# Performance work log

Hardware: AMD Instinct MI355X
Metric: run time of the kernel (lower is better)

Reference implementation:

```python
import jax, jax.numpy as jnp
import numpy as np

N_NODES = 50000
N_EDGES = 800000
D_IN = 128
D_OUT = 128


def _dedup_mask(src, dst, n_nodes):
    # True for exactly one representative edge per unique (src, dst) pair.
    # Equivalent to the torch unique() over cat(src_feat, dst) rows, since
    # distinct src nodes have distinct (random continuous) feature rows.
    key = src.astype(jnp.int64) * n_nodes + dst.astype(jnp.int64)
    order = jnp.argsort(key)
    ks = key[order]
    first = jnp.concatenate([jnp.array([True]), ks[1:] != ks[:-1]])
    mask = jnp.zeros(key.shape[0], dtype=bool).at[order].set(first)
    return mask


def setup_inputs() -> dict:
    key = jax.random.key(0)
    k1, k2, k3, k4, k5, k6, k7 = jax.random.split(key, 7)
    nfeats = jax.random.normal(k1, (N_NODES, D_IN), dtype=jnp.float32)
    src = jax.random.randint(k2, (N_EDGES,), 0, N_NODES, dtype=jnp.int64)
    dst = jax.random.randint(k3, (N_EDGES,), 0, N_NODES, dtype=jnp.int64)
    s1 = 1.0 / np.sqrt(D_IN)
    s2 = 1.0 / np.sqrt(D_OUT)
    W1 = jax.random.uniform(k4, (D_IN, D_OUT), jnp.float32, -s1, s1)
    b1 = jax.random.uniform(k5, (D_OUT,), jnp.float32, -s1, s1)
    W2 = jax.random.uniform(k6, (D_OUT, D_OUT), jnp.float32, -s2, s2)
    b2 = jax.random.uniform(k7, (D_OUT,), jnp.float32, -s2, s2)
    alpha = jnp.zeros((1,), dtype=jnp.float32)  # init_alpha=0, not learned
    return {"nfeats": nfeats, "src": src, "dst": dst,
            "W1": W1, "b1": b1, "W2": W2, "b2": b2, "alpha": alpha}


def reference(nfeats, src, dst, W1, b1, W2, b2, alpha):
    # message: gather src features, zero out duplicate (feat, dst) rows
    mask = _dedup_mask(src, dst, N_NODES)  # [E]
    m = nfeats[src] * mask[:, None].astype(nfeats.dtype)  # [E, D_IN]
    # sum aggregation into dst nodes
    agg = jax.ops.segment_sum(m, dst, num_segments=N_NODES)  # [N, D_IN]
    h = (1.0 + alpha[0]) * nfeats + agg
    # MLP (2 layers): Linear -> ReLU -> Linear (BatchNorms unused in source forward)
    h = jax.nn.relu(h @ W1 + b1)
    h = h @ W2 + b2
    # norm=None, act=None, dropout=0 -> identity
    return h
```

## Files before the change

### kernel.cpp

```cpp
#include <hip/hip_runtime.h>

typedef unsigned int u32;
typedef unsigned short u16;
typedef long long i64;

#define NNODES 50000
#define NEDGES 800000
#define DF 128
#define CAP 64
#define NBINS 196
#define BINCAP 5120
#define EPB 4096

typedef __bf16 bf16x8 __attribute__((ext_vector_type(8)));
typedef float f32x4 __attribute__((ext_vector_type(4)));

__device__ __forceinline__ u16 f2bf(float f) {
    union { float f; u32 i; } v; v.f = f;
    u32 u = v.i;
    return (u16)((u + 0x7fffu + ((u >> 16) & 1u)) >> 16);
}

__global__ __launch_bounds__(256) void detect_kernel(const u32* __restrict__ src_w,
                                                     u32* __restrict__ flag,
                                                     u32* __restrict__ cursors) {
    __shared__ int any_nz;
    cursors[threadIdx.x] = 0u;
    if (threadIdx.x == 0) any_nz = 0;
    __syncthreads();
    if (src_w[2 * threadIdx.x + 1] != 0u) atomicOr(&any_nz, 1);
    __syncthreads();
    if (threadIdx.x == 0) *flag = (any_nz == 0) ? 1u : 0u;
}

__global__ __launch_bounds__(256) void bin_kernel(const void* __restrict__ src,
                                                  const void* __restrict__ dst,
                                                  const u32* __restrict__ flag,
                                                  u32* __restrict__ cursors,
                                                  u32* __restrict__ binbuf) {
    __shared__ u32 s_cnt[NBINS];
    __shared__ u32 s_base[NBINS];
    int t = threadIdx.x;
    for (int i = t; i < NBINS; i += 256) s_cnt[i] = 0u;
    __syncthreads();

    bool is64 = (*flag != 0u);
    int e0 = blockIdx.x * EPB + t;
    u32 pk[16];
#pragma unroll
    for (int i = 0; i < 16; ++i) {
        int e = e0 + i * 256;
        pk[i] = 0xFFFFFFFFu;
        if (e < NEDGES) {
            int s, d;
            if (is64) { s = (int)((const i64*)src)[e]; d = (int)((const i64*)dst)[e]; }
            else      { s = ((const int*)src)[e];      d = ((const int*)dst)[e]; }
            pk[i] = (u32)s | ((u32)d << 16);
            atomicAdd(&s_cnt[(u32)d >> 8], 1u);
        }
    }
    __syncthreads();
    if (t < NBINS) {
        s_base[t] = atomicAdd(&cursors[t], s_cnt[t]);
        s_cnt[t] = 0u;
    }
    __syncthreads();
#pragma unroll
    for (int i = 0; i < 16; ++i) {
        if (pk[i] != 0xFFFFFFFFu) {
            u32 bin = pk[i] >> 24;
            u32 off = s_base[bin] + atomicAdd(&s_cnt[bin], 1u);
            if (off < BINCAP) binbuf[bin * BINCAP + off] = pk[i];
        }
    }
}

__global__ __launch_bounds__(256) void build_kernel(const u32* __restrict__ cursors,
                                                    const u32* __restrict__ binbuf,
                                                    u32* __restrict__ counts,
                                                    int* __restrict__ edge_src) {
    __shared__ u32 cnt[256];
    int t = threadIdx.x;
    cnt[t] = 0u;
    __syncthreads();
    int b = blockIdx.x;
    int n = (int)cursors[b]; if (n > BINCAP) n = BINCAP;
    for (int i = t; i < n; i += 256) {
        u32 pk = binbuf[b * BINCAP + i];
        int srcv = (int)(pk & 0xFFFFu);
        int dl = (int)((pk >> 16) & 0xFFu);
        u32 pos = atomicAdd(&cnt[dl], 1u);
        if (pos < CAP) edge_src[(((b << 8) + dl) << 6) + (int)pos] = srcv;
    }
    __syncthreads();
    counts[(b << 8) + t] = cnt[t];
}

__global__ __launch_bounds__(256) void gather_kernel(const float* __restrict__ nf,
                                                     const u32* __restrict__ counts,
                                                     const int* __restrict__ edge_src,
                                                     const float* __restrict__ alpha,
                                                     u16* __restrict__ X) {
    __shared__ __align__(16) int s_kept[4][CAP];
    int w = threadIdx.x >> 6, lane = threadIdx.x & 63;
    int d = blockIdx.x * 4 + w;
    int c = (int)counts[d];
    int cc = c < CAP ? c : CAP;

    float al = 1.0f + alpha[0];
    float2 dv = *(const float2*)(nf + (size_t)d * DF + 2 * lane);

    int si = 0;
    bool k = false;
    if (lane < cc) { si = edge_src[(d << 6) + lane]; k = true; }
    for (int j = 0; j < cc - 1; ++j) {
        int v = __shfl(si, j, 64);
        if (j < lane && v == si) k = false;
    }
    unsigned long long m = __ballot(k);
    if (k) s_kept[w][__popcll(m & ((1ull << lane) - 1ull))] = si;
    int nk = __popcll(m);
    __builtin_amdgcn_wave_barrier();

    float a0 = 0.f, a1 = 0.f;
    int i = 0;
    for (; i + 8 <= nk; i += 8) {
        int4 q0 = *(const int4*)&s_kept[w][i];
        int4 q1 = *(const int4*)&s_kept[w][i + 4];
        float2 v0 = *(const float2*)(nf + (size_t)q0.x * DF + 2 * lane);
        float2 v1 = *(const float2*)(nf + (size_t)q0.y * DF + 2 * lane);
        float2 v2 = *(const float2*)(nf + (size_t)q0.z * DF + 2 * lane);
        float2 v3 = *(const float2*)(nf + (size_t)q0.w * DF + 2 * lane);
        float2 v4 = *(const float2*)(nf + (size_t)q1.x * DF + 2 * lane);
        float2 v5 = *(const float2*)(nf + (size_t)q1.y * DF + 2 * lane);
        float2 v6 = *(const float2*)(nf + (size_t)q1.z * DF + 2 * lane);
        float2 v7 = *(const float2*)(nf + (size_t)q1.w * DF + 2 * lane);
        a0 += ((v0.x + v1.x) + (v2.x + v3.x)) + ((v4.x + v5.x) + (v6.x + v7.x));
        a1 += ((v0.y + v1.y) + (v2.y + v3.y)) + ((v4.y + v5.y) + (v6.y + v7.y));
    }
    for (; i + 4 <= nk; i += 4) {
        int4 q = *(const int4*)&s_kept[w][i];
        float2 v0 = *(const float2*)(nf + (size_t)q.x * DF + 2 * lane);
        float2 v1 = *(const float2*)(nf + (size_t)q.y * DF + 2 * lane);
        float2 v2 = *(const float2*)(nf + (size_t)q.z * DF + 2 * lane);
        float2 v3 = *(const float2*)(nf + (size_t)q.w * DF + 2 * lane);
        a0 += (v0.x + v1.x) + (v2.x + v3.x);
        a1 += (v0.y + v1.y) + (v2.y + v3.y);
    }
    for (; i < nk; ++i) {
        int s = s_kept[w][i];
        float2 v = *(const float2*)(nf + (size_t)s * DF + 2 * lane);
        a0 += v.x; a1 += v.y;
    }

    u32 pk = (u32)f2bf(fmaf(al, dv.x, a0)) | ((u32)f2bf(fmaf(al, dv.y, a1)) << 16);
    *(u32*)(X + (size_t)d * DF + 2 * lane) = pk;
}

__global__ __launch_bounds__(256) void wconv_kernel(const float* __restrict__ W1,
                                                    const float* __restrict__ W2,
                                                    u16* __restrict__ W1T,
                                                    u16* __restrict__ W2T) {
    int i = blockIdx.x * 256 + threadIdx.x;
    const float* W = (i < 16384) ? W1 : W2;
    u16* T = (i < 16384) ? W1T : W2T;
    int j = i & 16383;
    int n = j >> 7, k = j & 127;
    T[j] = f2bf(W[k * 128 + n]);
}

__global__ __launch_bounds__(256) void mlp_kernel(const u16* __restrict__ Xb,
                                                  const u16* __restrict__ W1T,
                                                  const float* __restrict__ b1,
                                                  const u16* __restrict__ W2T,
                                                  const float* __restrict__ b2,
                                                  float* __restrict__ O,
                                                  int M) {
    __shared__ __align__(16) u16 sA[64][136];
    __shared__ __align__(16) u16 sW[128][136];
    __shared__ float sB[128];

    const int tid = threadIdx.x;
    const int m0 = blockIdx.x * 64;
    const int wave = tid >> 6, lane = tid & 63;
    const int lrow = lane & 15, quad = lane >> 4;
    const int warow = wave * 16;

    for (int i = tid; i < 2048; i += 256) {
        int n = i >> 4, c8 = i & 15;
        *(uint4*)((char*)(&sW[0][0]) + n * 272 + c8 * 16) = ((const uint4*)W1T)[i];
    }
    if (tid < 128) sB[tid] = b1[tid];

    for (int i = tid; i < 1024; i += 256) {
        int r = i >> 4, c8 = i & 15;
        int gr = m0 + r;
        uint4 v = make_uint4(0u, 0u, 0u, 0u);
        if (gr < M) v = *(const uint4*)(Xb + (size_t)gr * DF + c8 * 8);
        *(uint4*)((char*)(&sA[0][0]) + r * 272 + c8 * 16) = v;
    }
    __syncthreads();

    {
        f32x4 acc[8];
#pragma unroll
        for (int nt = 0; nt < 8; ++nt) acc[nt] = (f32x4){0.f, 0.f, 0.f, 0.f};
#pragma unroll
        for (int kk = 0; kk < 4; ++kk) {
            bf16x8 a = *(const bf16x8*)((const char*)(&sA[0][0]) + (warow + lrow) * 272 + kk * 64 + quad * 16);
#pragma unroll
            for (int nt = 0; nt < 8; ++nt) {
                bf16x8 b = *(const bf16x8*)((const char*)(&sW[0][0]) + (nt * 16 + lrow) * 272 + kk * 64 + quad * 16);
                acc[nt] = __builtin_amdgcn_mfma_f32_16x16x32_bf16(a, b, acc[nt], 0, 0, 0);
            }
        }
#pragma unroll
        for (int nt = 0; nt < 8; ++nt) {
            int col = nt * 16 + lrow;
            float bc = sB[col];
#pragma unroll
            for (int r = 0; r < 4; ++r)
                sA[warow + quad * 4 + r][col] = f2bf(fmaxf(acc[nt][r] + bc, 0.0f));
        }
    }
    __syncthreads();

    for (int i = tid; i < 2048; i += 256) {
        int n = i >> 4, c8 = i & 15;
        *(uint4*)((char*)(&sW[0][0]) + n * 272 + c8 * 16) = ((const uint4*)W2T)[i];
    }
    if (tid < 128) sB[tid] = b2[tid];
    __syncthreads();

    {
        f32x4 acc[8];
#pragma unroll
        for (int nt = 0; nt < 8; ++nt) acc[nt] = (f32x4){0.f, 0.f, 0.f, 0.f};
#pragma unroll
        for (int kk = 0; kk < 4; ++kk) {
            bf16x8 a = *(const bf16x8*)((const char*)(&sA[0][0]) + (warow + lrow) * 272 + kk * 64 + quad * 16);
#pragma unroll
            for (int nt = 0; nt < 8; ++nt) {
                bf16x8 b = *(const bf16x8*)((const char*)(&sW[0][0]) + (nt * 16 + lrow) * 272 + kk * 64 + quad * 16);
                acc[nt] = __builtin_amdgcn_mfma_f32_16x16x32_bf16(a, b, acc[nt], 0, 0, 0);
            }
        }
#pragma unroll
        for (int nt = 0; nt < 8; ++nt) {
            int col = nt * 16 + lrow;
            float bc = sB[col];
#pragma unroll
            for (int r = 0; r < 4; ++r) {
                int grow = m0 + warow + quad * 4 + r;
                if (grow < M) O[(size_t)grow * DF + col] = acc[nt][r] + bc;
            }
        }
    }
}

extern "C" void kernel_launch(void* const* d_in, const int* in_sizes, int n_in,
                              void* d_out, int out_size, void* d_ws, size_t ws_size,
                              hipStream_t stream) {
    const float* nfeats = (const float*)d_in[0];
    const void*  src    = d_in[1];
    const void*  dst    = d_in[2];
    const float* W1     = (const float*)d_in[3];
    const float* b1     = (const float*)d_in[4];
    const float* W2     = (const float*)d_in[5];
    const float* b2     = (const float*)d_in[6];
    const float* alpha  = (const float*)d_in[7];

    char* ws = (char*)d_ws;
    u32* counts   = (u32*)ws;
    int* edge_src = (int*)(ws + 200704);
    u32* flag     = (u32*)(ws + 13000704);
    u16* W1T      = (u16*)(ws + 13000720);
    u16* W2T      = (u16*)(ws + 13033488);
    u16* X        = (u16*)(ws + 13066256);
    u32* binbuf   = (u32*)(ws + 13066256);
    u32* cursors  = (u32*)(ws + 25866256);

    detect_kernel<<<1, 256, 0, stream>>>((const u32*)src, flag, cursors);
    wconv_kernel<<<128, 256, 0, stream>>>(W1, W2, W1T, W2T);
    bin_kernel<<<(NEDGES + EPB - 1) / EPB, 256, 0, stream>>>(src, dst, flag, cursors, binbuf);
    build_kernel<<<NBINS, 256, 0, stream>>>(cursors, binbuf, counts, edge_src);
    gather_kernel<<<NNODES / 4, 256, 0, stream>>>(nfeats, counts, edge_src, alpha, X);
    mlp_kernel<<<(NNODES + 63) / 64, 256, 0, stream>>>(X, W1T, b1, W2T, b2, (float*)d_out, NNODES);
}
```

Measured before the change: 187.6 us.

## Fuse gather into MLP, store features in fp16, and split build per half-bin

```diff
diff --git a/kernel.cpp b/kernel.cpp
--- a/kernel.cpp
+++ b/kernel.cpp
@@ -10,27 +10,59 @@
 #define CAP 64
 #define NBINS 196
 #define BINCAP 5120
-#define EPB 4096
+#define EPB 2048
 
 typedef __bf16 bf16x8 __attribute__((ext_vector_type(8)));
 typedef float f32x4 __attribute__((ext_vector_type(4)));
+typedef _Float16 f16x2 __attribute__((ext_vector_type(2)));
 
 __device__ __forceinline__ u16 f2bf(float f) {
     union { float f; u32 i; } v; v.f = f;
     u32 u = v.i;
     return (u16)((u + 0x7fffu + ((u >> 16) & 1u)) >> 16);
 }
-
-__global__ __launch_bounds__(256) void detect_kernel(const u32* __restrict__ src_w,
-                                                     u32* __restrict__ flag,
-                                                     u32* __restrict__ cursors) {
-    __shared__ int any_nz;
-    cursors[threadIdx.x] = 0u;
-    if (threadIdx.x == 0) any_nz = 0;
-    __syncthreads();
-    if (src_w[2 * threadIdx.x + 1] != 0u) atomicOr(&any_nz, 1);
-    __syncthreads();
-    if (threadIdx.x == 0) *flag = (any_nz == 0) ? 1u : 0u;
+__device__ __forceinline__ u16 f2h(float f) {
+    _Float16 h = (_Float16)f;
+    union { _Float16 h; u16 u; } v; v.h = h;
+    return v.u;
+}
+__device__ __forceinline__ float2 h2f2(u32 w) {
+    union { u32 u; f16x2 h; } v; v.u = w;
+    return make_float2((float)v.h.x, (float)v.h.y);
+}
+
+__global__ __launch_bounds__(256) void prep_kernel(const float* __restrict__ nfeats,
+                                                   const float* __restrict__ W1,
+                                                   const float* __restrict__ W2,
+                                                   const u32* __restrict__ src_w,
+                                                   u16* __restrict__ nf16,
+                                                   u16* __restrict__ W1T,
+                                                   u16* __restrict__ W2T,
+                                                   u32* __restrict__ flag,
+                                                   u32* __restrict__ cursors) {
+    int bid = blockIdx.x, tid = threadIdx.x;
+    if (bid < 6250) {
+        int i = bid * 256 + tid;
+        float4 v = ((const float4*)nfeats)[i];
+        ushort4 o;
+        o.x = f2h(v.x); o.y = f2h(v.y); o.z = f2h(v.z); o.w = f2h(v.w);
+        ((ushort4*)nf16)[i] = o;
+    } else if (bid < 6378) {
+        int j = (bid - 6250) * 256 + tid;
+        const float* W = (j < 16384) ? W1 : W2;
+        u16* T = (j < 16384) ? W1T : W2T;
+        int jj = j & 16383;
+        int n = jj >> 7, k = jj & 127;
+        T[jj] = f2bf(W[k * 128 + n]);
+    } else {
+        __shared__ int any_nz;
+        for (int i = tid; i < NBINS * 16; i += 256) cursors[i] = 0u;
+        if (tid == 0) any_nz = 0;
+        __syncthreads();
+        if (src_w[2 * tid + 1] != 0u) atomicOr(&any_nz, 1);
+        __syncthreads();
+        if (tid == 0) *flag = (any_nz == 0) ? 1u : 0u;
+    }
 }
 
 __global__ __launch_bounds__(256) void bin_kernel(const void* __restrict__ src,
@@ -46,9 +78,9 @@
 
     bool is64 = (*flag != 0u);
     int e0 = blockIdx.x * EPB + t;
-    u32 pk[16];
-#pragma unroll
-    for (int i = 0; i < 16; ++i) {
+    u32 pk[8];
+#pragma unroll
+    for (int i = 0; i < 8; ++i) {
         int e = e0 + i * 256;
         pk[i] = 0xFFFFFFFFu;
         if (e < NEDGES) {
@@ -61,12 +93,12 @@
     }
     __syncthreads();
     if (t < NBINS) {
-        s_base[t] = atomicAdd(&cursors[t], s_cnt[t]);
+        s_base[t] = atomicAdd(&cursors[t * 16], s_cnt[t]);
         s_cnt[t] = 0u;
     }
     __syncthreads();
 #pragma unroll
-    for (int i = 0; i < 16; ++i) {
+    for (int i = 0; i < 8; ++i) {
         if (pk[i] != 0xFFFFFFFFu) {
             u32 bin = pk[i] >> 24;
             u32 off = s_base[bin] + atomicAdd(&s_cnt[bin], 1u);
@@ -78,107 +110,39 @@
 __global__ __launch_bounds__(256) void build_kernel(const u32* __restrict__ cursors,
                                                     const u32* __restrict__ binbuf,
                                                     u32* __restrict__ counts,
-                                                    int* __restrict__ edge_src) {
-    __shared__ u32 cnt[256];
+                                                    u16* __restrict__ edge16) {
+    __shared__ u32 cnt[128];
     int t = threadIdx.x;
-    cnt[t] = 0u;
-    __syncthreads();
-    int b = blockIdx.x;
-    int n = (int)cursors[b]; if (n > BINCAP) n = BINCAP;
+    if (t < 128) cnt[t] = 0u;
+    __syncthreads();
+    int b = blockIdx.x >> 1, half = blockIdx.x & 1;
+    int n = (int)cursors[b * 16]; if (n > BINCAP) n = BINCAP;
     for (int i = t; i < n; i += 256) {
         u32 pk = binbuf[b * BINCAP + i];
-        int srcv = (int)(pk & 0xFFFFu);
         int dl = (int)((pk >> 16) & 0xFFu);
-        u32 pos = atomicAdd(&cnt[dl], 1u);
-        if (pos < CAP) edge_src[(((b << 8) + dl) << 6) + (int)pos] = srcv;
-    }
-    __syncthreads();
-    counts[(b << 8) + t] = cnt[t];
-}
-
-__global__ __launch_bounds__(256) void gather_kernel(const float* __restrict__ nf,
-                                                     const u32* __restrict__ counts,
-                                                     const int* __restrict__ edge_src,
-                                                     const float* __restrict__ alpha,
-                                                     u16* __restrict__ X) {
-    __shared__ __align__(16) int s_kept[4][CAP];
-    int w = threadIdx.x >> 6, lane = threadIdx.x & 63;
-    int d = blockIdx.x * 4 + w;
-    int c = (int)counts[d];
-    int cc = c < CAP ? c : CAP;
-
-    float al = 1.0f + alpha[0];
-    float2 dv = *(const float2*)(nf + (size_t)d * DF + 2 * lane);
-
-    int si = 0;
-    bool k = false;
-    if (lane < cc) { si = edge_src[(d << 6) + lane]; k = true; }
-    for (int j = 0; j < cc - 1; ++j) {
-        int v = __shfl(si, j, 64);
-        if (j < lane && v == si) k = false;
-    }
-    unsigned long long m = __ballot(k);
-    if (k) s_kept[w][__popcll(m & ((1ull << lane) - 1ull))] = si;
-    int nk = __popcll(m);
-    __builtin_amdgcn_wave_barrier();
-
-    float a0 = 0.f, a1 = 0.f;
-    int i = 0;
-    for (; i + 8 <= nk; i += 8) {
-        int4 q0 = *(const int4*)&s_kept[w][i];
-        int4 q1 = *(const int4*)&s_kept[w][i + 4];
-        float2 v0 = *(const float2*)(nf + (size_t)q0.x * DF + 2 * lane);
-        float2 v1 = *(const float2*)(nf + (size_t)q0.y * DF + 2 * lane);
-        float2 v2 = *(const float2*)(nf + (size_t)q0.z * DF + 2 * lane);
-        float2 v3 = *(const float2*)(nf + (size_t)q0.w * DF + 2 * lane);
-        float2 v4 = *(const float2*)(nf + (size_t)q1.x * DF + 2 * lane);
-        float2 v5 = *(const float2*)(nf + (size_t)q1.y * DF + 2 * lane);
-        float2 v6 = *(const float2*)(nf + (size_t)q1.z * DF + 2 * lane);
-        float2 v7 = *(const float2*)(nf + (size_t)q1.w * DF + 2 * lane);
-        a0 += ((v0.x + v1.x) + (v2.x + v3.x)) + ((v4.x + v5.x) + (v6.x + v7.x));
-        a1 += ((v0.y + v1.y) + (v2.y + v3.y)) + ((v4.y + v5.y) + (v6.y + v7.y));
-    }
-    for (; i + 4 <= nk; i += 4) {
-        int4 q = *(const int4*)&s_kept[w][i];
-        float2 v0 = *(const float2*)(nf + (size_t)q.x * DF + 2 * lane);
-        float2 v1 = *(const float2*)(nf + (size_t)q.y * DF + 2 * lane);
-        float2 v2 = *(const float2*)(nf + (size_t)q.z * DF + 2 * lane);
-        float2 v3 = *(const float2*)(nf + (size_t)q.w * DF + 2 * lane);
-        a0 += (v0.x + v1.x) + (v2.x + v3.x);
-        a1 += (v0.y + v1.y) + (v2.y + v3.y);
-    }
-    for (; i < nk; ++i) {
-        int s = s_kept[w][i];
-        float2 v = *(const float2*)(nf + (size_t)s * DF + 2 * lane);
-        a0 += v.x; a1 += v.y;
-    }
-
-    u32 pk = (u32)f2bf(fmaf(al, dv.x, a0)) | ((u32)f2bf(fmaf(al, dv.y, a1)) << 16);
-    *(u32*)(X + (size_t)d * DF + 2 * lane) = pk;
-}
-
-__global__ __launch_bounds__(256) void wconv_kernel(const float* __restrict__ W1,
-                                                    const float* __restrict__ W2,
-                                                    u16* __restrict__ W1T,
-                                                    u16* __restrict__ W2T) {
-    int i = blockIdx.x * 256 + threadIdx.x;
-    const float* W = (i < 16384) ? W1 : W2;
-    u16* T = (i < 16384) ? W1T : W2T;
-    int j = i & 16383;
-    int n = j >> 7, k = j & 127;
-    T[j] = f2bf(W[k * 128 + n]);
-}
-
-__global__ __launch_bounds__(256) void mlp_kernel(const u16* __restrict__ Xb,
-                                                  const u16* __restrict__ W1T,
-                                                  const float* __restrict__ b1,
-                                                  const u16* __restrict__ W2T,
-                                                  const float* __restrict__ b2,
-                                                  float* __restrict__ O,
-                                                  int M) {
+        if ((dl >> 7) == half) {
+            u32 pos = atomicAdd(&cnt[dl & 127], 1u);
+            if (pos < CAP) edge16[(((b << 8) + dl) << 6) + (int)pos] = (u16)(pk & 0xFFFFu);
+        }
+    }
+    __syncthreads();
+    if (t < 128) counts[(b << 8) + half * 128 + t] = cnt[t];
+}
+
+__global__ __launch_bounds__(256) void fused_kernel(const u16* __restrict__ nf16,
+                                                    const u32* __restrict__ counts,
+                                                    const u16* __restrict__ edge16,
+                                                    const float* __restrict__ alpha,
+                                                    const u16* __restrict__ W1T,
+                                                    const float* __restrict__ b1,
+                                                    const u16* __restrict__ W2T,
+                                                    const float* __restrict__ b2,
+                                                    float* __restrict__ O,
+                                                    int M) {
     __shared__ __align__(16) u16 sA[64][136];
     __shared__ __align__(16) u16 sW[128][136];
     __shared__ float sB[128];
+    __shared__ __align__(16) u32 s_kept[4][CAP];
 
     const int tid = threadIdx.x;
     const int m0 = blockIdx.x * 64;
@@ -192,12 +156,66 @@
     }
     if (tid < 128) sB[tid] = b1[tid];
 
-    for (int i = tid; i < 1024; i += 256) {
-        int r = i >> 4, c8 = i & 15;
-        int gr = m0 + r;
-        uint4 v = make_uint4(0u, 0u, 0u, 0u);
-        if (gr < M) v = *(const uint4*)(Xb + (size_t)gr * DF + c8 * 8);
-        *(uint4*)((char*)(&sA[0][0]) + r * 272 + c8 * 16) = v;
+    float al = 1.0f + alpha[0];
+
+    for (int ii = 0; ii < 16; ++ii) {
+        int row = warow + ii;
+        int d = m0 + row;
+        u32 pkout = 0u;
+        if (d < M) {
+            int c = (int)counts[d];
+            int cc = c < CAP ? c : CAP;
+            u32 si = 0u; bool k = false;
+            if (lane < cc) { si = (u32)edge16[(d << 6) + lane]; k = true; }
+            for (int j = 0; j < cc - 1; ++j) {
+                u32 v = (u32)__shfl((int)si, j, 64);
+                if (j < lane && v == si) k = false;
+            }
+            unsigned long long m = __ballot(k);
+            if (k) s_kept[wave][__popcll(m & ((1ull << lane) - 1ull))] = si;
+            int nk = __popcll(m);
+            __builtin_amdgcn_wave_barrier();
+
+            float a0 = 0.f, a1 = 0.f;
+            int i = 0;
+            for (; i + 8 <= nk; i += 8) {
+                int4 q0 = *(const int4*)&s_kept[wave][i];
+                int4 q1 = *(const int4*)&s_kept[wave][i + 4];
+                u32 r0 = *(const u32*)(nf16 + (size_t)(u32)q0.x * DF + 2 * lane);
+                u32 r1 = *(const u32*)(nf16 + (size_t)(u32)q0.y * DF + 2 * lane);
+                u32 r2 = *(const u32*)(nf16 + (size_t)(u32)q0.z * DF + 2 * lane);
+                u32 r3 = *(const u32*)(nf16 + (size_t)(u32)q0.w * DF + 2 * lane);
+                u32 r4 = *(const u32*)(nf16 + (size_t)(u32)q1.x * DF + 2 * lane);
+                u32 r5 = *(const u32*)(nf16 + (size_t)(u32)q1.y * DF + 2 * lane);
+                u32 r6 = *(const u32*)(nf16 + (size_t)(u32)q1.z * DF + 2 * lane);
+                u32 r7 = *(const u32*)(nf16 + (size_t)(u32)q1.w * DF + 2 * lane);
+                float2 v0 = h2f2(r0), v1 = h2f2(r1), v2 = h2f2(r2), v3 = h2f2(r3);
+                float2 v4 = h2f2(r4), v5 = h2f2(r5), v6 = h2f2(r6), v7 = h2f2(r7);
+                a0 += ((v0.x + v1.x) + (v2.x + v3.x)) + ((v4.x + v5.x) + (v6.x + v7.x));
+                a1 += ((v0.y + v1.y) + (v2.y + v3.y)) + ((v4.y + v5.y) + (v6.y + v7.y));
+            }
+            for (; i + 4 <= nk; i += 4) {
+                int4 q = *(const int4*)&s_kept[wave][i];
+                u32 r0 = *(const u32*)(nf16 + (size_t)(u32)q.x * DF + 2 * lane);
+                u32 r1 = *(const u32*)(nf16 + (size_t)(u32)q.y * DF + 2 * lane);
+                u32 r2 = *(const u32*)(nf16 + (size_t)(u32)q.z * DF + 2 * lane);
+                u32 r3 = *(const u32*)(nf16 + (size_t)(u32)q.w * DF + 2 * lane);
+                float2 v0 = h2f2(r0), v1 = h2f2(r1), v2 = h2f2(r2), v3 = h2f2(r3);
+                a0 += (v0.x + v1.x) + (v2.x + v3.x);
+                a1 += (v0.y + v1.y) + (v2.y + v3.y);
+            }
+            for (; i < nk; ++i) {
+                u32 r = *(const u32*)(nf16 + (size_t)s_kept[wave][i] * DF + 2 * lane);
+                float2 v = h2f2(r);
+                a0 += v.x; a1 += v.y;
+            }
+            __builtin_amdgcn_wave_barrier();
+
+            u32 rd = *(const u32*)(nf16 + (size_t)d * DF + 2 * lane);
+            float2 dv = h2f2(rd);
+            pkout = (u32)f2bf(fmaf(al, dv.x, a0)) | ((u32)f2bf(fmaf(al, dv.y, a1)) << 16);
+        }
+        *(u32*)((char*)(&sA[0][0]) + row * 272 + 4 * lane) = pkout;
     }
     __syncthreads();
 
@@ -272,18 +290,19 @@
 
     char* ws = (char*)d_ws;
     u32* counts   = (u32*)ws;
-    int* edge_src = (int*)(ws + 200704);
-    u32* flag     = (u32*)(ws + 13000704);
-    u16* W1T      = (u16*)(ws + 13000720);
-    u16* W2T      = (u16*)(ws + 13033488);
-    u16* X        = (u16*)(ws + 13066256);
-    u32* binbuf   = (u32*)(ws + 13066256);
-    u32* cursors  = (u32*)(ws + 25866256);
-
-    detect_kernel<<<1, 256, 0, stream>>>((const u32*)src, flag, cursors);
-    wconv_kernel<<<128, 256, 0, stream>>>(W1, W2, W1T, W2T);
+    u16* edge16   = (u16*)(ws + 200704);
+    u32* flag     = (u32*)(ws + 6623232);
+    u16* W1T      = (u16*)(ws + 6623248);
+    u16* W2T      = (u16*)(ws + 6656016);
+    u16* nf16     = (u16*)(ws + 6688784);
+    u32* binbuf   = (u32*)(ws + 19488784);
+    u32* cursors  = (u32*)(ws + 23502864);
+
+    prep_kernel<<<6379, 256, 0, stream>>>(nfeats, W1, W2, (const u32*)src,
+                                          nf16, W1T, W2T, flag, cursors);
     bin_kernel<<<(NEDGES + EPB - 1) / EPB, 256, 0, stream>>>(src, dst, flag, cursors, binbuf);
-    build_kernel<<<NBINS, 256, 0, stream>>>(cursors, binbuf, counts, edge_src);
-    gather_kernel<<<NNODES / 4, 256, 0, stream>>>(nfeats, counts, edge_src, alpha, X);
-    mlp_kernel<<<(NNODES + 63) / 64, 256, 0, stream>>>(X, W1T, b1, W2T, b2, (float*)d_out, NNODES);
-}
+    build_kernel<<<NBINS * 2, 256, 0, stream>>>(cursors, binbuf, counts, edge16);
+    fused_kernel<<<(NNODES + 63) / 64, 256, 0, stream>>>(nf16, counts, edge16, alpha,
+                                                         W1T, b1, W2T, b2,
+                                                         (float*)d_out, NNODES);
+}
```

New measurement: 225.5 us. 1.2x slower.
